# Kernel tuning notes

Measured on AMD Instinct MI355X. Metric: run time of the kernel, lower is better.

Reference implementation:

```python
import jax, jax.numpy as jnp
import numpy as np
import math

EMBED_DIM = 1024
N_HEADS = 16
HEAD_DIM = EMBED_DIM // N_HEADS
NUM_CLASSES = 1000


def setup_inputs() -> dict:
    key = jax.random.key(0)
    k_x, k_wi, k_bi, k_wo, k_bo = jax.random.split(key, 5)
    bs, seq_len = 2, 2048
    x = jax.random.normal(k_x, (bs, seq_len, EMBED_DIM), dtype=jnp.float32)
    # torch.nn.Linear default init: U(-1/sqrt(fan_in), 1/sqrt(fan_in))
    bi = 1.0 / math.sqrt(EMBED_DIM)
    W_in = jax.random.uniform(k_wi, (EMBED_DIM, EMBED_DIM), minval=-bi, maxval=bi, dtype=jnp.float32)
    b_in = jax.random.uniform(k_bi, (EMBED_DIM,), minval=-bi, maxval=bi, dtype=jnp.float32)
    W_out = jax.random.uniform(k_wo, (NUM_CLASSES, EMBED_DIM), minval=-bi, maxval=bi, dtype=jnp.float32)
    b_out = jax.random.uniform(k_bo, (NUM_CLASSES,), minval=-bi, maxval=bi, dtype=jnp.float32)
    return {"x": x, "W_in": W_in, "b_in": b_in, "W_out": W_out, "b_out": b_out}


def reference(x, W_in, b_in, W_out, b_out):
    bs, seq_len, f = x.shape
    # input projection: x @ W_in^T + b_in
    p = jnp.einsum('bsf,gf->bsg', x, W_in) + b_in           # [bs, seq, embed]
    p = p.reshape(bs, seq_len, N_HEADS, HEAD_DIM)            # [bs, seq, h, d]
    p = jnp.transpose(p, (0, 2, 1, 3))                        # [bs, h, seq, d]
    scale = 1.0 / math.sqrt(f)                                # note: sqrt(embed_dim), not head_dim
    attn = jnp.einsum('bhqd,bhkd->bhqk', p, p) * scale        # [bs, h, seq, seq], no softmax
    vals = jnp.einsum('bhqk,bhkd->bhqd', attn, p)             # [bs, h, seq, d]
    vals = jnp.transpose(vals, (0, 2, 1, 3)).reshape(bs, seq_len, f)
    out = jnp.einsum('bsf,cf->bsc', vals, W_out) + b_out      # [bs, seq, num_classes]
    return out
```

## Files before the change

kernel.cpp:

```cpp
#include <hip/hip_runtime.h>
#include <hip/hip_bf16.h>
#include <cstdint>

#define EMBED   1024
#define NHEADS  16
#define HDIM    64
#define SEQ     2048
#define BSZ     2
#define MTOT    (BSZ*SEQ)
#define NCLS    1000
#define NPAD    1024

typedef __attribute__((ext_vector_type(8))) short short8;
typedef __attribute__((ext_vector_type(4))) short short4v;
typedef __attribute__((ext_vector_type(4))) float float4v;

typedef __attribute__((address_space(3))) unsigned lds_uint;
typedef __attribute__((address_space(1))) const unsigned gbl_uint;

__device__ __forceinline__ void gl2lds16(const void* g, void* l) {
    __builtin_amdgcn_global_load_lds((gbl_uint*)g, (lds_uint*)l, 16, 0, 0);
}

#define WAITVM6() asm volatile("s_waitcnt vmcnt(6)" ::: "memory")
#define WAITVM0() asm volatile("s_waitcnt vmcnt(0)" ::: "memory")
#define BAR()     asm volatile("s_barrier" ::: "memory")

__device__ __forceinline__ void storeC(float* p, float v) { *p = v; }
__device__ __forceinline__ void storeC(__hip_bfloat16* p, float v) { *p = __float2bfloat16(v); }

__device__ __forceinline__ unsigned packbf2(float a, float b) {
    __hip_bfloat16 ha = __float2bfloat16(a), hb = __float2bfloat16(b);
    unsigned short ua, ub;
    __builtin_memcpy(&ua, &ha, 2); __builtin_memcpy(&ub, &hb, 2);
    return (unsigned)ua | ((unsigned)ub << 16);
}
__device__ __forceinline__ short8 lds8u(const __hip_bfloat16* p) {
    union { uint2 u[2]; short8 s; } v;
    v.u[0] = *(const uint2*)p;
    v.u[1] = *(const uint2*)(p + 4);
    return v.s;
}

#define XN4  ((MTOT*EMBED)/4)
#define WN4  ((EMBED*EMBED)/4)
#define GN4  (32*64*64/4)
__global__ __launch_bounds__(256)
void conv_inputs(const float* __restrict__ x, const float* __restrict__ Win,
                 __hip_bfloat16* __restrict__ xb, __hip_bfloat16* __restrict__ Winb,
                 float* __restrict__ G) {
    const long i4 = (long)blockIdx.x * 256 + threadIdx.x;
    if (i4 < GN4)
        *(float4v*)(G + i4 * 4) = (float4v){0.f, 0.f, 0.f, 0.f};
    float4v v;
    __hip_bfloat16* dst;
    if (i4 < XN4) {
        v = *(const float4v*)(x + i4 * 4);
        dst = xb + i4 * 4;
    } else {
        const long j = i4 - XN4;
        v = *(const float4v*)(Win + j * 4);
        dst = Winb + j * 4;
    }
    short4v o;
#pragma unroll
    for (int u = 0; u < 4; u++)
        ((__hip_bfloat16*)&o)[u] = __float2bfloat16(v[u]);
    *(short4v*)dst = o;
}

template <typename CT, bool DO_GRAM>
__global__ __launch_bounds__(256)
void gemm_bt_bias(const __hip_bfloat16* __restrict__ A,
                  const __hip_bfloat16* __restrict__ B,
                  const float* __restrict__ bias,
                  CT* __restrict__ C,
                  float* __restrict__ G,
                  int K, int nstore, int cstride, long bstride) {
    __shared__ __hip_bfloat16 As[2][128 * 64];
    __shared__ __hip_bfloat16 Bs[2][64 * 64];

    const int t    = threadIdx.x;
    const int blk  = blockIdx.x;
    const int xcd  = blk & 7;
    const int j    = blk >> 3;
    const int bm   = (xcd * 4 + (j & 3)) * 128;
    const int bn   = (j >> 2) * 64;
    const __hip_bfloat16* Bb = B + (long)(bm >> 11) * bstride;
    const int wave = t >> 6, lane = t & 63;
    const int wm   = (wave & 1) * 64, wn = (wave >> 1) * 32;
    const int lrow = lane & 15, lq = lane >> 4;

    const __hip_bfloat16* Arow[4];
    const __hip_bfloat16* Brow[2];
#pragma unroll
    for (int i = 0; i < 4; i++) {
        const int ci = i * 256 + t;
        const int r  = ci >> 3;
        const int sc = ((ci & 7) ^ (r & 7)) * 8;
        Arow[i] = A + (long)(bm + r) * K + sc;
    }
#pragma unroll
    for (int i = 0; i < 2; i++) {
        const int ci = i * 256 + t;
        const int r  = ci >> 3;
        const int sc = ((ci & 7) ^ (r & 7)) * 8;
        Brow[i] = Bb + (long)(bn + r) * K + sc;
    }

    float4v acc[4][2];
#pragma unroll
    for (int i = 0; i < 4; i++)
#pragma unroll
        for (int jj = 0; jj < 2; jj++) acc[i][jj] = (float4v){0.f, 0.f, 0.f, 0.f};

    const int nIter = K >> 6;

#define STAGE_TILE(k0, buf)                                                     \
    do {                                                                        \
        _Pragma("unroll")                                                       \
        for (int i = 0; i < 4; i++)                                             \
            gl2lds16(Arow[i] + (k0), (char*)As[buf] + (i * 256 + t) * 16);      \
        _Pragma("unroll")                                                       \
        for (int i = 0; i < 2; i++)                                             \
            gl2lds16(Brow[i] + (k0), (char*)Bs[buf] + (i * 256 + t) * 16);      \
    } while (0)

    STAGE_TILE(0, 0);

    for (int it = 0; it < nIter; ++it) {
        const int cur = it & 1, nxt = cur ^ 1;
        if (it + 1 < nIter) {
            STAGE_TILE((it + 1) << 6, nxt);
            WAITVM6();
        } else {
            WAITVM0();
        }
        BAR();

        const __hip_bfloat16* Ac = As[cur];
        const __hip_bfloat16* Bc = Bs[cur];
#pragma unroll
        for (int kk = 0; kk < 2; kk++) {
            short8 af[4], bf[2];
#pragma unroll
            for (int i = 0; i < 4; i++) {
                const int row = wm + i * 16 + lrow;
                const int sc  = (kk * 4 + lq) ^ (row & 7);
                af[i] = *(const short8*)(Ac + row * 64 + sc * 8);
            }
#pragma unroll
            for (int jj = 0; jj < 2; jj++) {
                const int row = wn + jj * 16 + lrow;
                const int sc  = (kk * 4 + lq) ^ (row & 7);
                bf[jj] = *(const short8*)(Bc + row * 64 + sc * 8);
            }
#pragma unroll
            for (int i = 0; i < 4; i++)
#pragma unroll
                for (int jj = 0; jj < 2; jj++)
                    acc[i][jj] = __builtin_amdgcn_mfma_f32_16x16x32_bf16(af[i], bf[jj], acc[i][jj], 0, 0, 0);
        }
        BAR();
    }
#undef STAGE_TILE

    float bv[2];
#pragma unroll
    for (int jj = 0; jj < 2; jj++) {
        const int gn = bn + wn + jj * 16 + lrow;
        bv[jj] = (gn < nstore) ? bias[gn] : 0.f;
    }

    if (DO_GRAM) {
        __hip_bfloat16* Pt = (__hip_bfloat16*)As;
#pragma unroll
        for (int i = 0; i < 4; i++) {
            const int m0 = wm + i * 16 + lq * 4;
#pragma unroll
            for (int jj = 0; jj < 2; jj++) {
                const int n = wn + jj * 16 + lrow;
                unsigned* dst = (unsigned*)(Pt + n * 132 + m0);
                dst[0] = packbf2(acc[i][jj][0] + bv[jj], acc[i][jj][1] + bv[jj]);
                dst[1] = packbf2(acc[i][jj][2] + bv[jj], acc[i][jj][3] + bv[jj]);
            }
        }
        __syncthreads();
    }

#pragma unroll
    for (int i = 0; i < 4; i++) {
        const int gm0 = bm + wm + i * 16 + lq * 4;
#pragma unroll
        for (int jj = 0; jj < 2; jj++) {
            const int gn = bn + wn + jj * 16 + lrow;
            if (gn < nstore) {
#pragma unroll
                for (int r = 0; r < 4; r++)
                    storeC(&C[(long)(gm0 + r) * cstride + gn], acc[i][jj][r] + bv[jj]);
            }
        }
    }

    if (DO_GRAM) {
        const __hip_bfloat16* Pt = (const __hip_bfloat16*)As;
        float4v g4[4];
#pragma unroll
        for (int t2 = 0; t2 < 4; t2++) g4[t2] = (float4v){0.f, 0.f, 0.f, 0.f};
        const int d1l = wave * 16 + lrow;
#pragma unroll
        for (int k0 = 0; k0 < 128; k0 += 32) {
            short8 af = lds8u(Pt + d1l * 132 + k0 + lq * 8);
#pragma unroll
            for (int t2 = 0; t2 < 4; t2++) {
                short8 bfr = lds8u(Pt + (t2 * 16 + lrow) * 132 + k0 + lq * 8);
                g4[t2] = __builtin_amdgcn_mfma_f32_16x16x32_bf16(af, bfr, g4[t2], 0, 0, 0);
            }
        }
        float* Gh = G + (long)((bm >> 11) * 16 + (bn >> 6)) * 4096;
        const int d1b = wave * 16 + lq * 4;
#pragma unroll
        for (int t2 = 0; t2 < 4; t2++) {
            const int d2 = t2 * 16 + lrow;
#pragma unroll
            for (int r = 0; r < 4; r++)
                atomicAdd(&Gh[(d1b + r) * 64 + d2], g4[t2][r]);
        }
    }
}

__global__ __launch_bounds__(256)
void weff_kernel(const float* __restrict__ Wout, const float* __restrict__ G,
                 __hip_bfloat16* __restrict__ WeffT) {
    const int n0 = blockIdx.x * 64;
    const int h  = blockIdx.y;
    const int b  = blockIdx.z;
    const float* Gh = G + (b * 16 + h) * 4096;

    __shared__ __hip_bfloat16 Wl[64 * 72];
    __shared__ __hip_bfloat16 Gl[64 * 72];
    const int t = threadIdx.x;

#pragma unroll
    for (int it = 0; it < 4; it++) {
        const int ci = it * 256 + t;
        const int r = ci >> 4, c4 = (ci & 15) * 4;
        float4v v = (float4v){0.f, 0.f, 0.f, 0.f};
        if (n0 + r < NCLS)
            v = *(const float4v*)(Wout + (long)(n0 + r) * EMBED + h * HDIM + c4);
        *(uint2*)(Wl + r * 72 + c4) = (uint2){packbf2(v[0], v[1]), packbf2(v[2], v[3])};
        float4v g = *(const float4v*)(Gh + r * 64 + c4);
        *(uint2*)(Gl + r * 72 + c4) = (uint2){packbf2(g[0], g[1]), packbf2(g[2], g[3])};
    }
    __syncthreads();

    const int wave = t >> 6, lane = t & 63;
    const int lrow = lane & 15, lq = lane >> 4;
    float4v acc[4];
#pragma unroll
    for (int jj = 0; jj < 4; jj++) acc[jj] = (float4v){0.f, 0.f, 0.f, 0.f};

#pragma unroll
    for (int k0 = 0; k0 < 64; k0 += 32) {
        short8 af = *(const short8*)(Wl + (wave * 16 + lrow) * 72 + k0 + lq * 8);
#pragma unroll
        for (int jj = 0; jj < 4; jj++) {
            short8 bfr = *(const short8*)(Gl + (jj * 16 + lrow) * 72 + k0 + lq * 8);
            acc[jj] = __builtin_amdgcn_mfma_f32_16x16x32_bf16(af, bfr, acc[jj], 0, 0, 0);
        }
    }

    const float scale = 1.0f / 32.0f;
    __hip_bfloat16* Wt = WeffT + (long)b * EMBED * NPAD;
#pragma unroll
    for (int jj = 0; jj < 4; jj++) {
        const int d1 = jj * 16 + lrow;
#pragma unroll
        for (int r = 0; r < 4; r++) {
            const int n = n0 + wave * 16 + lq * 4 + r;
            Wt[(long)n * EMBED + h * HDIM + d1] = __float2bfloat16(acc[jj][r] * scale);
        }
    }
}

extern "C" void kernel_launch(void* const* d_in, const int* in_sizes, int n_in,
                              void* d_out, int out_size, void* d_ws, size_t ws_size,
                              hipStream_t stream) {
    const float* x     = (const float*)d_in[0];
    const float* W_in  = (const float*)d_in[1];
    const float* b_in  = (const float*)d_in[2];
    const float* W_out = (const float*)d_in[3];
    const float* b_out = (const float*)d_in[4];
    float* out = (float*)d_out;

    char* ws = (char*)d_ws;
    __hip_bfloat16* xb    = (__hip_bfloat16*)(ws);
    __hip_bfloat16* Winb  = (__hip_bfloat16*)(ws + (8u  << 20));
    __hip_bfloat16* P     = (__hip_bfloat16*)(ws + (10u << 20));
    float*          G     = (float*)(ws + (18u << 20));
    __hip_bfloat16* WeffT = (__hip_bfloat16*)(ws + (19u << 20));

    conv_inputs<<<(XN4 + WN4) / 256, 256, 0, stream>>>(x, W_in, xb, Winb, G);
    gemm_bt_bias<__hip_bfloat16, true><<<512, 256, 0, stream>>>(
        xb, Winb, b_in, P, G, EMBED, NPAD, NPAD, 0);
    weff_kernel<<<dim3(16, 16, 2), 256, 0, stream>>>(W_out, G, WeffT);
    gemm_bt_bias<float, false><<<512, 256, 0, stream>>>(
        P, WeffT, b_out, out, nullptr, EMBED, NCLS, NCLS, (long)EMBED * NPAD);
}
```

Measured before the change: 123.1 us.

## Replace LDS-staged GEMM mainloop with direct global-to-register prefetch pipeline

The GEMM main loop no longer stages A and B tiles through double-buffered LDS with barriers. Each wave now loads its MFMA fragments directly from global memory into registers, keeping four K-steps in flight. This removes LDS round trips and block-wide synchronisation. In exchange, global loads are duplicated across waves that share rows, and per-lane accesses are less coalesced. LDS shrinks to just the transpose buffer used by the Gram epilogue.

```diff
diff --git a/kernel.cpp b/kernel.cpp
--- a/kernel.cpp
+++ b/kernel.cpp
@@ -14,17 +14,6 @@
 typedef __attribute__((ext_vector_type(8))) short short8;
 typedef __attribute__((ext_vector_type(4))) short short4v;
 typedef __attribute__((ext_vector_type(4))) float float4v;
-
-typedef __attribute__((address_space(3))) unsigned lds_uint;
-typedef __attribute__((address_space(1))) const unsigned gbl_uint;
-
-__device__ __forceinline__ void gl2lds16(const void* g, void* l) {
-    __builtin_amdgcn_global_load_lds((gbl_uint*)g, (lds_uint*)l, 16, 0, 0);
-}
-
-#define WAITVM6() asm volatile("s_waitcnt vmcnt(6)" ::: "memory")
-#define WAITVM0() asm volatile("s_waitcnt vmcnt(0)" ::: "memory")
-#define BAR()     asm volatile("s_barrier" ::: "memory")
 
 __device__ __forceinline__ void storeC(float* p, float v) { *p = v; }
 __device__ __forceinline__ void storeC(__hip_bfloat16* p, float v) { *p = __float2bfloat16(v); }
@@ -76,9 +65,8 @@
                   const float* __restrict__ bias,
                   CT* __restrict__ C,
                   float* __restrict__ G,
-                  int K, int nstore, int cstride, long bstride) {
-    __shared__ __hip_bfloat16 As[2][128 * 64];
-    __shared__ __hip_bfloat16 Bs[2][64 * 64];
+                  int nstore, int cstride, long bstride) {
+    __shared__ __hip_bfloat16 Pt[64 * 132];
 
     const int t    = threadIdx.x;
     const int blk  = blockIdx.x;
@@ -91,22 +79,14 @@
     const int wm   = (wave & 1) * 64, wn = (wave >> 1) * 32;
     const int lrow = lane & 15, lq = lane >> 4;
 
-    const __hip_bfloat16* Arow[4];
-    const __hip_bfloat16* Brow[2];
-#pragma unroll
-    for (int i = 0; i < 4; i++) {
-        const int ci = i * 256 + t;
-        const int r  = ci >> 3;
-        const int sc = ((ci & 7) ^ (r & 7)) * 8;
-        Arow[i] = A + (long)(bm + r) * K + sc;
-    }
-#pragma unroll
-    for (int i = 0; i < 2; i++) {
-        const int ci = i * 256 + t;
-        const int r  = ci >> 3;
-        const int sc = ((ci & 7) ^ (r & 7)) * 8;
-        Brow[i] = Bb + (long)(bn + r) * K + sc;
-    }
+    const __hip_bfloat16* ap[4];
+    const __hip_bfloat16* bp[2];
+#pragma unroll
+    for (int i = 0; i < 4; i++)
+        ap[i] = A + (long)(bm + wm + i * 16 + lrow) * EMBED + lq * 8;
+#pragma unroll
+    for (int i = 0; i < 2; i++)
+        bp[i] = Bb + (long)(bn + wn + i * 16 + lrow) * EMBED + lq * 8;
 
     float4v acc[4][2];
 #pragma unroll
@@ -114,56 +94,40 @@
 #pragma unroll
         for (int jj = 0; jj < 2; jj++) acc[i][jj] = (float4v){0.f, 0.f, 0.f, 0.f};
 
-    const int nIter = K >> 6;
-
-#define STAGE_TILE(k0, buf)                                                     \
-    do {                                                                        \
-        _Pragma("unroll")                                                       \
-        for (int i = 0; i < 4; i++)                                             \
-            gl2lds16(Arow[i] + (k0), (char*)As[buf] + (i * 256 + t) * 16);      \
-        _Pragma("unroll")                                                       \
-        for (int i = 0; i < 2; i++)                                             \
-            gl2lds16(Brow[i] + (k0), (char*)Bs[buf] + (i * 256 + t) * 16);      \
+#define LOADG(AD, BD, koff)                                                      \
+    do {                                                                         \
+        _Pragma("unroll")                                                        \
+        for (int i = 0; i < 4; i++) (AD)[i] = *(const short8*)(ap[i] + (koff));  \
+        _Pragma("unroll")                                                        \
+        for (int i = 0; i < 2; i++) (BD)[i] = *(const short8*)(bp[i] + (koff));  \
     } while (0)
 
-    STAGE_TILE(0, 0);
-
-    for (int it = 0; it < nIter; ++it) {
-        const int cur = it & 1, nxt = cur ^ 1;
-        if (it + 1 < nIter) {
-            STAGE_TILE((it + 1) << 6, nxt);
-            WAITVM6();
-        } else {
-            WAITVM0();
-        }
-        BAR();
-
-        const __hip_bfloat16* Ac = As[cur];
-        const __hip_bfloat16* Bc = Bs[cur];
-#pragma unroll
-        for (int kk = 0; kk < 2; kk++) {
-            short8 af[4], bf[2];
-#pragma unroll
-            for (int i = 0; i < 4; i++) {
-                const int row = wm + i * 16 + lrow;
-                const int sc  = (kk * 4 + lq) ^ (row & 7);
-                af[i] = *(const short8*)(Ac + row * 64 + sc * 8);
-            }
-#pragma unroll
-            for (int jj = 0; jj < 2; jj++) {
-                const int row = wn + jj * 16 + lrow;
-                const int sc  = (kk * 4 + lq) ^ (row & 7);
-                bf[jj] = *(const short8*)(Bc + row * 64 + sc * 8);
-            }
-#pragma unroll
-            for (int i = 0; i < 4; i++)
-#pragma unroll
-                for (int jj = 0; jj < 2; jj++)
-                    acc[i][jj] = __builtin_amdgcn_mfma_f32_16x16x32_bf16(af[i], bf[jj], acc[i][jj], 0, 0, 0);
-        }
-        BAR();
-    }
-#undef STAGE_TILE
+#define MFMA_STEP(AD, BD)                                                        \
+    do {                                                                         \
+        _Pragma("unroll")                                                        \
+        for (int i = 0; i < 4; i++)                                              \
+            _Pragma("unroll")                                                    \
+            for (int jj = 0; jj < 2; jj++)                                       \
+                acc[i][jj] = __builtin_amdgcn_mfma_f32_16x16x32_bf16(            \
+                    (AD)[i], (BD)[jj], acc[i][jj], 0, 0, 0);                     \
+    } while (0)
+
+    short8 a[4][4];
+    short8 b[4][2];
+    LOADG(a[0], b[0], 0);
+    LOADG(a[1], b[1], 32);
+    LOADG(a[2], b[2], 64);
+    LOADG(a[3], b[3], 96);
+
+#pragma unroll
+    for (int s = 0; s < 32; s += 4) {
+        MFMA_STEP(a[0], b[0]); if (s + 4 < 32) LOADG(a[0], b[0], (s + 4) * 32);
+        MFMA_STEP(a[1], b[1]); if (s + 5 < 32) LOADG(a[1], b[1], (s + 5) * 32);
+        MFMA_STEP(a[2], b[2]); if (s + 6 < 32) LOADG(a[2], b[2], (s + 6) * 32);
+        MFMA_STEP(a[3], b[3]); if (s + 7 < 32) LOADG(a[3], b[3], (s + 7) * 32);
+    }
+#undef LOADG
+#undef MFMA_STEP
 
     float bv[2];
 #pragma unroll
@@ -173,7 +137,6 @@
     }
 
     if (DO_GRAM) {
-        __hip_bfloat16* Pt = (__hip_bfloat16*)As;
 #pragma unroll
         for (int i = 0; i < 4; i++) {
             const int m0 = wm + i * 16 + lq * 4;
@@ -203,7 +166,6 @@
     }
 
     if (DO_GRAM) {
-        const __hip_bfloat16* Pt = (const __hip_bfloat16*)As;
         float4v g4[4];
 #pragma unroll
         for (int t2 = 0; t2 < 4; t2++) g4[t2] = (float4v){0.f, 0.f, 0.f, 0.f};
@@ -302,8 +264,8 @@
 
     conv_inputs<<<(XN4 + WN4) / 256, 256, 0, stream>>>(x, W_in, xb, Winb, G);
     gemm_bt_bias<__hip_bfloat16, true><<<512, 256, 0, stream>>>(
-        xb, Winb, b_in, P, G, EMBED, NPAD, NPAD, 0);
+        xb, Winb, b_in, P, G, NPAD, NPAD, 0);
     weff_kernel<<<dim3(16, 16, 2), 256, 0, stream>>>(W_out, G, WeffT);
     gemm_bt_bias<float, false><<<512, 256, 0, stream>>>(
-        P, WeffT, b_out, out, nullptr, EMBED, NCLS, NCLS, (long)EMBED * NPAD);
-}
+        P, WeffT, b_out, out, nullptr, NCLS, NCLS, (long)EMBED * NPAD);
+}
```

New measurement: 182.5 us. 1.48x slower.

## Split Gram computation into separate kernel and shrink GEMM tiles to 64x64

Applied to the files above, without the earlier changes.

Removes the fused Gram-matrix epilogue, with its float atomics, from the input-projection GEMM and computes per-head Gram partials in a new gram64 kernel that writes two halves summed later in weff_kernel. Both GEMMs now use 64x64 tiles on 1024 blocks with a launch-bounds occupancy hint, where they used 128x64 tiles on 512 blocks. This also drops the G zeroing from the conversion kernel. In exchange it adds a kernel launch, rereads P from memory, and the gram64 grid of only 64 blocks does a serial 16-chunk loop with scalar LDS transposes.

```diff
diff --git a/kernel.cpp b/kernel.cpp
--- a/kernel.cpp
+++ b/kernel.cpp
@@ -22,7 +22,7 @@
     __builtin_amdgcn_global_load_lds((gbl_uint*)g, (lds_uint*)l, 16, 0, 0);
 }
 
-#define WAITVM6() asm volatile("s_waitcnt vmcnt(6)" ::: "memory")
+#define WAITVM4() asm volatile("s_waitcnt vmcnt(4)" ::: "memory")
 #define WAITVM0() asm volatile("s_waitcnt vmcnt(0)" ::: "memory")
 #define BAR()     asm volatile("s_barrier" ::: "memory")
 
@@ -44,14 +44,10 @@
 
 #define XN4  ((MTOT*EMBED)/4)
 #define WN4  ((EMBED*EMBED)/4)
-#define GN4  (32*64*64/4)
 __global__ __launch_bounds__(256)
 void conv_inputs(const float* __restrict__ x, const float* __restrict__ Win,
-                 __hip_bfloat16* __restrict__ xb, __hip_bfloat16* __restrict__ Winb,
-                 float* __restrict__ G) {
+                 __hip_bfloat16* __restrict__ xb, __hip_bfloat16* __restrict__ Winb) {
     const long i4 = (long)blockIdx.x * 256 + threadIdx.x;
-    if (i4 < GN4)
-        *(float4v*)(G + i4 * 4) = (float4v){0.f, 0.f, 0.f, 0.f};
     float4v v;
     __hip_bfloat16* dst;
     if (i4 < XN4) {
@@ -69,57 +65,50 @@
     *(short4v*)dst = o;
 }
 
-template <typename CT, bool DO_GRAM>
-__global__ __launch_bounds__(256)
+template <typename CT>
+__global__ __launch_bounds__(256, 4)
 void gemm_bt_bias(const __hip_bfloat16* __restrict__ A,
                   const __hip_bfloat16* __restrict__ B,
                   const float* __restrict__ bias,
                   CT* __restrict__ C,
-                  float* __restrict__ G,
-                  int K, int nstore, int cstride, long bstride) {
-    __shared__ __hip_bfloat16 As[2][128 * 64];
+                  int nstore, int cstride, long bstride) {
+    __shared__ __hip_bfloat16 As[2][64 * 64];
     __shared__ __hip_bfloat16 Bs[2][64 * 64];
 
     const int t    = threadIdx.x;
     const int blk  = blockIdx.x;
     const int xcd  = blk & 7;
     const int j    = blk >> 3;
-    const int bm   = (xcd * 4 + (j & 3)) * 128;
-    const int bn   = (j >> 2) * 64;
+    const int bm   = (xcd * 8 + (j & 7)) * 64;
+    const int bn   = (j >> 3) * 64;
     const __hip_bfloat16* Bb = B + (long)(bm >> 11) * bstride;
     const int wave = t >> 6, lane = t & 63;
-    const int wm   = (wave & 1) * 64, wn = (wave >> 1) * 32;
+    const int wm   = (wave & 1) * 32, wn = (wave >> 1) * 32;
     const int lrow = lane & 15, lq = lane >> 4;
 
-    const __hip_bfloat16* Arow[4];
+    const __hip_bfloat16* Arow[2];
     const __hip_bfloat16* Brow[2];
-#pragma unroll
-    for (int i = 0; i < 4; i++) {
-        const int ci = i * 256 + t;
-        const int r  = ci >> 3;
-        const int sc = ((ci & 7) ^ (r & 7)) * 8;
-        Arow[i] = A + (long)(bm + r) * K + sc;
-    }
 #pragma unroll
     for (int i = 0; i < 2; i++) {
         const int ci = i * 256 + t;
         const int r  = ci >> 3;
         const int sc = ((ci & 7) ^ (r & 7)) * 8;
-        Brow[i] = Bb + (long)(bn + r) * K + sc;
-    }
-
-    float4v acc[4][2];
-#pragma unroll
-    for (int i = 0; i < 4; i++)
+        Arow[i] = A  + (long)(bm + r) * EMBED + sc;
+        Brow[i] = Bb + (long)(bn + r) * EMBED + sc;
+    }
+
+    float4v acc[2][2];
+#pragma unroll
+    for (int i = 0; i < 2; i++)
 #pragma unroll
         for (int jj = 0; jj < 2; jj++) acc[i][jj] = (float4v){0.f, 0.f, 0.f, 0.f};
 
-    const int nIter = K >> 6;
+    const int nIter = EMBED >> 6;
 
 #define STAGE_TILE(k0, buf)                                                     \
     do {                                                                        \
         _Pragma("unroll")                                                       \
-        for (int i = 0; i < 4; i++)                                             \
+        for (int i = 0; i < 2; i++)                                             \
             gl2lds16(Arow[i] + (k0), (char*)As[buf] + (i * 256 + t) * 16);      \
         _Pragma("unroll")                                                       \
         for (int i = 0; i < 2; i++)                                             \
@@ -132,7 +121,7 @@
         const int cur = it & 1, nxt = cur ^ 1;
         if (it + 1 < nIter) {
             STAGE_TILE((it + 1) << 6, nxt);
-            WAITVM6();
+            WAITVM4();
         } else {
             WAITVM0();
         }
@@ -142,9 +131,9 @@
         const __hip_bfloat16* Bc = Bs[cur];
 #pragma unroll
         for (int kk = 0; kk < 2; kk++) {
-            short8 af[4], bf[2];
-#pragma unroll
-            for (int i = 0; i < 4; i++) {
+            short8 af[2], bf[2];
+#pragma unroll
+            for (int i = 0; i < 2; i++) {
                 const int row = wm + i * 16 + lrow;
                 const int sc  = (kk * 4 + lq) ^ (row & 7);
                 af[i] = *(const short8*)(Ac + row * 64 + sc * 8);
@@ -156,7 +145,7 @@
                 bf[jj] = *(const short8*)(Bc + row * 64 + sc * 8);
             }
 #pragma unroll
-            for (int i = 0; i < 4; i++)
+            for (int i = 0; i < 2; i++)
 #pragma unroll
                 for (int jj = 0; jj < 2; jj++)
                     acc[i][jj] = __builtin_amdgcn_mfma_f32_16x16x32_bf16(af[i], bf[jj], acc[i][jj], 0, 0, 0);
@@ -171,25 +160,8 @@
         const int gn = bn + wn + jj * 16 + lrow;
         bv[jj] = (gn < nstore) ? bias[gn] : 0.f;
     }
-
-    if (DO_GRAM) {
-        __hip_bfloat16* Pt = (__hip_bfloat16*)As;
-#pragma unroll
-        for (int i = 0; i < 4; i++) {
-            const int m0 = wm + i * 16 + lq * 4;
-#pragma unroll
-            for (int jj = 0; jj < 2; jj++) {
-                const int n = wn + jj * 16 + lrow;
-                unsigned* dst = (unsigned*)(Pt + n * 132 + m0);
-                dst[0] = packbf2(acc[i][jj][0] + bv[jj], acc[i][jj][1] + bv[jj]);
-                dst[1] = packbf2(acc[i][jj][2] + bv[jj], acc[i][jj][3] + bv[jj]);
-            }
-        }
-        __syncthreads();
-    }
-
-#pragma unroll
-    for (int i = 0; i < 4; i++) {
+#pragma unroll
+    for (int i = 0; i < 2; i++) {
         const int gm0 = bm + wm + i * 16 + lq * 4;
 #pragma unroll
         for (int jj = 0; jj < 2; jj++) {
@@ -201,41 +173,68 @@
             }
         }
     }
-
-    if (DO_GRAM) {
-        const __hip_bfloat16* Pt = (const __hip_bfloat16*)As;
-        float4v g4[4];
-#pragma unroll
-        for (int t2 = 0; t2 < 4; t2++) g4[t2] = (float4v){0.f, 0.f, 0.f, 0.f};
-        const int d1l = wave * 16 + lrow;
-#pragma unroll
-        for (int k0 = 0; k0 < 128; k0 += 32) {
-            short8 af = lds8u(Pt + d1l * 132 + k0 + lq * 8);
+}
+
+__global__ __launch_bounds__(256)
+void gram64(const __hip_bfloat16* __restrict__ P, float* __restrict__ Gpart) {
+    __shared__ __hip_bfloat16 Pt[64 * 68];
+    const int t    = threadIdx.x;
+    const int blk  = blockIdx.x;
+    const int bh   = blk >> 1;
+    const int half = blk & 1;
+    const int b    = bh >> 4, h = bh & 15;
+    const int row0 = b * SEQ + half * 1024;
+
+    const int wave = t >> 6, lane = t & 63;
+    const int lrow = lane & 15, lq = lane >> 4;
+
+    float4v g4[4];
+#pragma unroll
+    for (int t2 = 0; t2 < 4; t2++) g4[t2] = (float4v){0.f, 0.f, 0.f, 0.f};
+
+    for (int c = 0; c < 16; c++) {
+#pragma unroll
+        for (int i = 0; i < 2; i++) {
+            const int ci = i * 256 + t;
+            const int r = ci >> 3, c8 = (ci & 7) * 8;
+            short8 v = *(const short8*)(P + (long)(row0 + c * 64 + r) * EMBED + h * HDIM + c8);
+#pragma unroll
+            for (int u = 0; u < 8; u++)
+                Pt[(c8 + u) * 68 + r] = ((const __hip_bfloat16*)&v)[u];
+        }
+        __syncthreads();
+
+#pragma unroll
+        for (int k0 = 0; k0 < 64; k0 += 32) {
+            short8 af = lds8u(Pt + (wave * 16 + lrow) * 68 + k0 + lq * 8);
 #pragma unroll
             for (int t2 = 0; t2 < 4; t2++) {
-                short8 bfr = lds8u(Pt + (t2 * 16 + lrow) * 132 + k0 + lq * 8);
+                short8 bfr = lds8u(Pt + (t2 * 16 + lrow) * 68 + k0 + lq * 8);
                 g4[t2] = __builtin_amdgcn_mfma_f32_16x16x32_bf16(af, bfr, g4[t2], 0, 0, 0);
             }
         }
-        float* Gh = G + (long)((bm >> 11) * 16 + (bn >> 6)) * 4096;
-        const int d1b = wave * 16 + lq * 4;
-#pragma unroll
-        for (int t2 = 0; t2 < 4; t2++) {
-            const int d2 = t2 * 16 + lrow;
-#pragma unroll
-            for (int r = 0; r < 4; r++)
-                atomicAdd(&Gh[(d1b + r) * 64 + d2], g4[t2][r]);
-        }
+        __syncthreads();
+    }
+
+    float* Gh = Gpart + (long)blk * 4096;
+    const int d1b = wave * 16 + lq * 4;
+#pragma unroll
+    for (int t2 = 0; t2 < 4; t2++) {
+        const int d2 = t2 * 16 + lrow;
+#pragma unroll
+        for (int r = 0; r < 4; r++)
+            Gh[(d1b + r) * 64 + d2] = g4[t2][r];
     }
 }
 
 __global__ __launch_bounds__(256)
-void weff_kernel(const float* __restrict__ Wout, const float* __restrict__ G,
+void weff_kernel(const float* __restrict__ Wout, const float* __restrict__ Gpart,
                  __hip_bfloat16* __restrict__ WeffT) {
     const int n0 = blockIdx.x * 64;
     const int h  = blockIdx.y;
     const int b  = blockIdx.z;
-    const float* Gh = G + (b * 16 + h) * 4096;
+    const float* G0 = Gpart + (long)((b * 16 + h) * 2 + 0) * 4096;
+    const float* G1 = Gpart + (long)((b * 16 + h) * 2 + 1) * 4096;
 
     __shared__ __hip_bfloat16 Wl[64 * 72];
     __shared__ __hip_bfloat16 Gl[64 * 72];
@@ -249,8 +248,11 @@
         if (n0 + r < NCLS)
             v = *(const float4v*)(Wout + (long)(n0 + r) * EMBED + h * HDIM + c4);
         *(uint2*)(Wl + r * 72 + c4) = (uint2){packbf2(v[0], v[1]), packbf2(v[2], v[3])};
-        float4v g = *(const float4v*)(Gh + r * 64 + c4);
-        *(uint2*)(Gl + r * 72 + c4) = (uint2){packbf2(g[0], g[1]), packbf2(g[2], g[3])};
+        float4v g0 = *(const float4v*)(G0 + r * 64 + c4);
+        float4v g1 = *(const float4v*)(G1 + r * 64 + c4);
+        *(uint2*)(Gl + r * 72 + c4) =
+            (uint2){packbf2(g0[0] + g1[0], g0[1] + g1[1]),
+                    packbf2(g0[2] + g1[2], g0[3] + g1[3])};
     }
     __syncthreads();
 
@@ -297,13 +299,14 @@
     __hip_bfloat16* xb    = (__hip_bfloat16*)(ws);
     __hip_bfloat16* Winb  = (__hip_bfloat16*)(ws + (8u  << 20));
     __hip_bfloat16* P     = (__hip_bfloat16*)(ws + (10u << 20));
-    float*          G     = (float*)(ws + (18u << 20));
-    __hip_bfloat16* WeffT = (__hip_bfloat16*)(ws + (19u << 20));
-
-    conv_inputs<<<(XN4 + WN4) / 256, 256, 0, stream>>>(x, W_in, xb, Winb, G);
-    gemm_bt_bias<__hip_bfloat16, true><<<512, 256, 0, stream>>>(
-        xb, Winb, b_in, P, G, EMBED, NPAD, NPAD, 0);
-    weff_kernel<<<dim3(16, 16, 2), 256, 0, stream>>>(W_out, G, WeffT);
-    gemm_bt_bias<float, false><<<512, 256, 0, stream>>>(
-        P, WeffT, b_out, out, nullptr, EMBED, NCLS, NCLS, (long)EMBED * NPAD);
-}
+    float*          Gpart = (float*)(ws + (18u << 20));
+    __hip_bfloat16* WeffT = (__hip_bfloat16*)(ws + (20u << 20));
+
+    conv_inputs<<<(XN4 + WN4) / 256, 256, 0, stream>>>(x, W_in, xb, Winb);
+    gemm_bt_bias<__hip_bfloat16><<<1024, 256, 0, stream>>>(
+        xb, Winb, b_in, P, NPAD, NPAD, 0);
+    gram64<<<64, 256, 0, stream>>>(P, Gpart);
+    weff_kernel<<<dim3(16, 16, 2), 256, 0, stream>>>(W_out, Gpart, WeffT);
+    gemm_bt_bias<float><<<1024, 256, 0, stream>>>(
+        P, WeffT, b_out, out, NCLS, NCLS, (long)EMBED * NPAD);
+}
```

Measured after the change: 127.2 us. +3.4%, slower.
